# Optimization experiments

Hardware: AMD Instinct MI355X
Metric: run time of the kernel (lower is better)

The kernel has to match this reference:

```python
import jax, jax.numpy as jnp
import numpy as np

EPS = 1e-06
NUM_HEADS = 16


def _rms_norm(x, g, eps=EPS):
    # normalize over the last (full model) dim, as WanRMSNorm(dim)
    var = jnp.mean(jnp.square(x), axis=-1, keepdims=True)
    return x * jax.lax.rsqrt(var + eps) * g


def _apply_rope(q, k, freqs):
    # q, k: [b, s, n, d]; freqs: [s, d//2] angles. Interleaved (complex) pairs
    b, s, n, d = q.shape
    cos = jnp.cos(freqs)[None, :, None, :]  # [1, s, 1, d//2]
    sin = jnp.sin(freqs)[None, :, None, :]

    def rot(t):
        tr = t.reshape(b, s, n, d // 2, 2)
        t0, t1 = tr[..., 0], tr[..., 1]
        o0 = t0 * cos - t1 * sin
        o1 = t0 * sin + t1 * cos
        return jnp.stack([o0, o1], axis=-1).reshape(b, s, n, d)

    return rot(q), rot(k)


def setup_inputs() -> dict:
    key = jax.random.key(0)
    ks = jax.random.split(key, 8)
    b, s, dim = 2, 2048, 2048
    hd = dim // NUM_HEADS
    x = jax.random.normal(ks[0], (b, s, dim), dtype=jnp.float32)
    seq_lens = jax.random.randint(ks[1], (b,), s // 2, s + 1, dtype=jnp.int32)
    grid_sizes = jax.random.randint(ks[2], (b, 3), 1, 16).astype(jnp.int64)
    freqs = jax.random.uniform(ks[3], (s, hd // 2), dtype=jnp.float32) * 6.283
    sc = 1.0 / np.sqrt(dim)
    Wq = jax.random.normal(ks[4], (dim, dim), dtype=jnp.float32) * sc
    Wk = jax.random.normal(ks[5], (dim, dim), dtype=jnp.float32) * sc
    Wv = jax.random.normal(ks[6], (dim, dim), dtype=jnp.float32) * sc
    Wo = jax.random.normal(ks[7], (dim, dim), dtype=jnp.float32) * sc
    bo = jnp.zeros((dim,), dtype=jnp.float32)
    gq = jnp.ones((dim,), dtype=jnp.float32)
    gk = jnp.ones((dim,), dtype=jnp.float32)
    return {"x": x, "seq_lens": seq_lens, "grid_sizes": grid_sizes, "freqs": freqs,
            "Wq": Wq, "Wk": Wk, "Wv": Wv, "Wo": Wo, "bo": bo, "gq": gq, "gk": gk}


def reference(x, seq_lens, grid_sizes, freqs, Wq, Wk, Wv, Wo, bo, gq, gk):
    b, s, dim = x.shape
    n = NUM_HEADS
    d = dim // n
    scale = d ** (-0.5)

    # QKV projections (Linear: x @ W.T), with RMSNorm over full dim on q/k
    q = _rms_norm(x @ Wq.T, gq).reshape(b, s, n, d)
    k = _rms_norm(x @ Wk.T, gk).reshape(b, s, n, d)
    v = (x @ Wv.T).reshape(b, s, n, d)

    q, k = _apply_rope(q, k, freqs)

    # varlen attention: keys beyond seq_lens[b] are masked out
    scores = jnp.einsum("bqnd,bknd->bnqk", q, k) * scale
    key_valid = jnp.arange(s)[None, None, None, :] < seq_lens[:, None, None, None]
    scores = jnp.where(key_valid, scores, jnp.float32(-1e9))
    probs = jax.nn.softmax(scores, axis=-1)
    attn = jnp.einsum("bnqk,bknd->bqnd", probs, v).reshape(b, s, dim)

    return attn @ Wo.T + bo
```

## Files before the change

kernel.cpp:

```cpp
#include <hip/hip_runtime.h>
#include <hip/hip_bf16.h>
#include <math.h>

#define BATCH 2
#define SEQ   2048
#define DIM   2048
#define NH    16
#define HD    128
#define NROWS (BATCH * SEQ)
#define EPS_RMS 1e-6f

typedef unsigned short ushort_t;
typedef unsigned int   uint_t;
typedef __bf16    bf16x8 __attribute__((ext_vector_type(8)));
typedef _Float16  f16x8  __attribute__((ext_vector_type(8)));
typedef float     f32x4  __attribute__((ext_vector_type(4)));

__device__ inline ushort_t f2bf(float f) {
    uint_t u = __builtin_bit_cast(uint_t, f);
    uint_t r = u + 0x7FFFu + ((u >> 16) & 1u);
    return (ushort_t)(r >> 16);
}
__device__ inline ushort_t f2h(float f) {
    return __builtin_bit_cast(ushort_t, (_Float16)f);
}

__global__ __launch_bounds__(256) void cvt_all_kernel(
    const float* __restrict__ x,  const float* __restrict__ wq,
    const float* __restrict__ wk, const float* __restrict__ wv,
    const float* __restrict__ wo,
    ushort_t* __restrict__ xh,  ushort_t* __restrict__ wqh,
    ushort_t* __restrict__ wkh, ushort_t* __restrict__ wvh,
    ushort_t* __restrict__ woh)
{
    const int blk = blockIdx.x;
    const float* src; ushort_t* dst; size_t base;
    if (blk < 4096) { src = x; dst = xh; base = (size_t)blk * 2048; }
    else {
        const int r = blk - 4096;
        const int wsel = r >> 11;
        base = (size_t)(r & 2047) * 2048;
        if      (wsel == 0) { src = wq; dst = wqh; }
        else if (wsel == 1) { src = wk; dst = wkh; }
        else if (wsel == 2) { src = wv; dst = wvh; }
        else                { src = wo; dst = woh; }
    }
    const size_t i = base + ((size_t)threadIdx.x << 3);
    float v[8];
    *(float4*)&v[0] = *(const float4*)&src[i];
    *(float4*)&v[4] = *(const float4*)&src[i + 4];
    uint_t pk[4];
#pragma unroll
    for (int j = 0; j < 4; ++j)
        pk[j] = (uint_t)f2h(v[2 * j]) | ((uint_t)f2h(v[2 * j + 1]) << 16);
    *(uint4*)&dst[i] = make_uint4(pk[0], pk[1], pk[2], pk[3]);
}

template<int MODE>
__global__ __launch_bounds__(256, 2) void gemm_f16_kernel(
    const ushort_t* __restrict__ Ah, const ushort_t* __restrict__ Bh,
    const float* __restrict__ bias,
    float* __restrict__ C, ushort_t* __restrict__ Ct,
    const int M, const int N, const int K)
{
    __shared__ __align__(16) ushort_t sA[4096], sB[4096];
    const int tid  = threadIdx.x;
    const int w    = tid >> 6;
    const int lane = tid & 63;
    const int m0 = blockIdx.y * 128;
    const int n0 = blockIdx.x * 128;

    const int scol = (lane & 3) << 3;
    const int wr = w >> 1, wc = w & 1;
    const int fr = lane & 15, quad = lane >> 4;

    f32x4 acc[4][4];
#pragma unroll
    for (int mi = 0; mi < 4; ++mi)
#pragma unroll
        for (int ni = 0; ni < 4; ++ni)
            acc[mi][ni] = (f32x4){0.f, 0.f, 0.f, 0.f};

    for (int k0 = 0; k0 < K; k0 += 32) {
        __syncthreads();
#pragma unroll
        for (int it = 0; it < 2; ++it) {
            const int row  = (w << 5) + (it << 4) + (lane >> 2);
            const int loff = (w << 10) + (it << 9);
            const size_t ga = (size_t)(m0 + row) * K + k0 + scol;
            const size_t gb = (size_t)(n0 + row) * K + k0 + scol;
            __builtin_amdgcn_global_load_lds(
                (const __attribute__((address_space(1))) uint_t*)(const void*)(Ah + ga),
                (__attribute__((address_space(3))) uint_t*)(void*)&sA[loff], 16, 0, 0);
            __builtin_amdgcn_global_load_lds(
                (const __attribute__((address_space(1))) uint_t*)(const void*)(Bh + gb),
                (__attribute__((address_space(3))) uint_t*)(void*)&sB[loff], 16, 0, 0);
        }
        __syncthreads();

        f16x8 bfr[4];
#pragma unroll
        for (int ni = 0; ni < 4; ++ni) {
            const int row = (wc << 6) + (ni << 4) + fr;
            bfr[ni] = *(const f16x8*)&sB[(row << 5) + (quad << 3)];
        }
#pragma unroll
        for (int mi = 0; mi < 4; ++mi) {
            const int row = (wr << 6) + (mi << 4) + fr;
            const f16x8 ah = *(const f16x8*)&sA[(row << 5) + (quad << 3)];
#pragma unroll
            for (int ni = 0; ni < 4; ++ni)
                acc[mi][ni] = __builtin_amdgcn_mfma_f32_16x16x32_f16(ah, bfr[ni], acc[mi][ni], 0, 0, 0);
        }
    }

#pragma unroll
    for (int mi = 0; mi < 4; ++mi)
#pragma unroll
        for (int ni = 0; ni < 4; ++ni) {
            const int col = n0 + (wc << 6) + (ni << 4) + fr;
            if (MODE == 0) {
                const float bv = bias ? bias[col] : 0.f;
#pragma unroll
                for (int r = 0; r < 4; ++r) {
                    const int rowg = m0 + (wr << 6) + (mi << 4) + (quad << 2) + r;
                    C[(size_t)rowg * N + col] = acc[mi][ni][r] + bv;
                }
            } else {
                const int rowg = m0 + (wr << 6) + (mi << 4) + (quad << 2);
                const int bb = rowg >> 11, tok = rowg & (SEQ - 1);
                const int hh = col >> 7, d = col & (HD - 1);
                uint2 pk;
                pk.x = (uint_t)f2bf(acc[mi][ni][0]) | ((uint_t)f2bf(acc[mi][ni][1]) << 16);
                pk.y = (uint_t)f2bf(acc[mi][ni][2]) | ((uint_t)f2bf(acc[mi][ni][3]) << 16);
                *(uint2*)&Ct[((size_t)(bb * NH + hh) * HD + d) * SEQ + tok] = pk;
            }
        }
}

__global__ __launch_bounds__(256, 3) void qkv_gemm_kernel(
    const ushort_t* __restrict__ Ah, const ushort_t* __restrict__ Bq,
    const ushort_t* __restrict__ Bk, const ushort_t* __restrict__ Bv,
    float* __restrict__ Qb, float* __restrict__ Kb, ushort_t* __restrict__ Vt)
{
    __shared__ __align__(16) ushort_t sA[4096], sB[4096];
    const int tid  = threadIdx.x;
    const int w    = tid >> 6;
    const int lane = tid & 63;

    const int bid = blockIdx.x;
    const int nid = (bid & 7) * 192 + (bid >> 3);
    const int n_blk = nid >> 5;
    const int m_blk = nid & 31;
    const int wsel  = n_blk >> 4;
    const int m0 = m_blk * 128;
    const int n0 = (n_blk & 15) * 128;
    const ushort_t* __restrict__ Bh = (wsel == 0) ? Bq : (wsel == 1) ? Bk : Bv;

    const int scol = (lane & 3) << 3;
    const int wr = w >> 1, wc = w & 1;
    const int fr = lane & 15, quad = lane >> 4;

    f32x4 acc[4][4];
#pragma unroll
    for (int mi = 0; mi < 4; ++mi)
#pragma unroll
        for (int ni = 0; ni < 4; ++ni)
            acc[mi][ni] = (f32x4){0.f, 0.f, 0.f, 0.f};

    for (int k0 = 0; k0 < DIM; k0 += 32) {
        __syncthreads();
#pragma unroll
        for (int it = 0; it < 2; ++it) {
            const int row  = (w << 5) + (it << 4) + (lane >> 2);
            const int loff = (w << 10) + (it << 9);
            const size_t ga = (size_t)(m0 + row) * DIM + k0 + scol;
            const size_t gb = (size_t)(n0 + row) * DIM + k0 + scol;
            __builtin_amdgcn_global_load_lds(
                (const __attribute__((address_space(1))) uint_t*)(const void*)(Ah + ga),
                (__attribute__((address_space(3))) uint_t*)(void*)&sA[loff], 16, 0, 0);
            __builtin_amdgcn_global_load_lds(
                (const __attribute__((address_space(1))) uint_t*)(const void*)(Bh + gb),
                (__attribute__((address_space(3))) uint_t*)(void*)&sB[loff], 16, 0, 0);
        }
        __syncthreads();

        f16x8 bfr[4];
#pragma unroll
        for (int ni = 0; ni < 4; ++ni) {
            const int row = (wc << 6) + (ni << 4) + fr;
            bfr[ni] = *(const f16x8*)&sB[(row << 5) + (quad << 3)];
        }
#pragma unroll
        for (int mi = 0; mi < 4; ++mi) {
            const int row = (wr << 6) + (mi << 4) + fr;
            const f16x8 ah = *(const f16x8*)&sA[(row << 5) + (quad << 3)];
#pragma unroll
            for (int ni = 0; ni < 4; ++ni)
                acc[mi][ni] = __builtin_amdgcn_mfma_f32_16x16x32_f16(ah, bfr[ni], acc[mi][ni], 0, 0, 0);
        }
    }

    if (wsel < 2) {
        float* __restrict__ C = (wsel == 0) ? Qb : Kb;
#pragma unroll
        for (int mi = 0; mi < 4; ++mi)
#pragma unroll
            for (int ni = 0; ni < 4; ++ni) {
                const int col = n0 + (wc << 6) + (ni << 4) + fr;
#pragma unroll
                for (int r = 0; r < 4; ++r) {
                    const int rowg = m0 + (wr << 6) + (mi << 4) + (quad << 2) + r;
                    C[(size_t)rowg * DIM + col] = acc[mi][ni][r];
                }
            }
    } else {
#pragma unroll
        for (int mi = 0; mi < 4; ++mi)
#pragma unroll
            for (int ni = 0; ni < 4; ++ni) {
                const int col = n0 + (wc << 6) + (ni << 4) + fr;
                const int rowg = m0 + (wr << 6) + (mi << 4) + (quad << 2);
                const int bb = rowg >> 11, tok = rowg & (SEQ - 1);
                const int hh = col >> 7, d = col & (HD - 1);
                uint2 pk;
                pk.x = (uint_t)f2bf(acc[mi][ni][0]) | ((uint_t)f2bf(acc[mi][ni][1]) << 16);
                pk.y = (uint_t)f2bf(acc[mi][ni][2]) | ((uint_t)f2bf(acc[mi][ni][3]) << 16);
                *(uint2*)&Vt[((size_t)(bb * NH + hh) * HD + d) * SEQ + tok] = pk;
            }
    }
}

#define BM 64
#define BN 64
#define BK 16

__global__ __launch_bounds__(256) void gemm_nt_kernel(
    const float* __restrict__ A, const float* __restrict__ W,
    const float* __restrict__ bias, float* __restrict__ C,
    const int M, const int N, const int K)
{
    __shared__ float As[BK][BM + 4];
    __shared__ float Bs[BK][BN + 4];
    const int tid = threadIdx.x;
    const int tx = tid & 15;
    const int ty = tid >> 4;
    const int m0 = blockIdx.y * BM;
    const int n0 = blockIdx.x * BN;
    const int ldr = tid >> 2;
    const int ldc = (tid & 3) << 2;

    float acc[4][4] = {};

    for (int k0 = 0; k0 < K; k0 += BK) {
        __syncthreads();
        const float4 av = *(const float4*)&A[(size_t)(m0 + ldr) * K + (k0 + ldc)];
        const float4 wv = *(const float4*)&W[(size_t)(n0 + ldr) * K + (k0 + ldc)];
        As[ldc + 0][ldr] = av.x; As[ldc + 1][ldr] = av.y;
        As[ldc + 2][ldr] = av.z; As[ldc + 3][ldr] = av.w;
        Bs[ldc + 0][ldr] = wv.x; Bs[ldc + 1][ldr] = wv.y;
        Bs[ldc + 2][ldr] = wv.z; Bs[ldc + 3][ldr] = wv.w;
        __syncthreads();
#pragma unroll
        for (int k = 0; k < BK; ++k) {
            const float4 a4 = *(const float4*)&As[k][ty << 2];
            const float4 b4 = *(const float4*)&Bs[k][tx << 2];
            const float aa[4] = {a4.x, a4.y, a4.z, a4.w};
            const float bb[4] = {b4.x, b4.y, b4.z, b4.w};
#pragma unroll
            for (int i = 0; i < 4; ++i)
#pragma unroll
                for (int j = 0; j < 4; ++j)
                    acc[i][j] = fmaf(aa[i], bb[j], acc[i][j]);
        }
    }

#pragma unroll
    for (int i = 0; i < 4; ++i) {
        const int row = m0 + (ty << 2) + i;
        const int col = n0 + (tx << 2);
        float4 ov;
        ov.x = acc[i][0]; ov.y = acc[i][1]; ov.z = acc[i][2]; ov.w = acc[i][3];
        if (bias != nullptr) {
            ov.x += bias[col + 0]; ov.y += bias[col + 1];
            ov.z += bias[col + 2]; ov.w += bias[col + 3];
        }
        *(float4*)&C[(size_t)row * N + col] = ov;
    }
}

__global__ __launch_bounds__(256) void rmsnorm_rope_qk_kernel(
    const float* __restrict__ Qb, const float* __restrict__ gq,
    ushort_t* __restrict__ qbh,
    const float* __restrict__ Kb, const float* __restrict__ gk,
    ushort_t* __restrict__ kbh,
    const float* __restrict__ freqs)
{
    const int r = blockIdx.x;
    const int s = r & (SEQ - 1);
    const int tid = threadIdx.x;
    const int base = tid << 3;
    const bool isQ = (blockIdx.y == 0);
    const float* T = isQ ? Qb : Kb;
    const float* g = isQ ? gq : gk;
    ushort_t* out  = isQ ? qbh : kbh;
    const float posc = isQ ? 0.088388347648318447f : 1.0f;

    float v[8];
    *(float4*)&v[0] = *(const float4*)&T[(size_t)r * DIM + base];
    *(float4*)&v[4] = *(const float4*)&T[(size_t)r * DIM + base + 4];

    float ss = 0.f;
#pragma unroll
    for (int i = 0; i < 8; ++i) ss += v[i] * v[i];
#pragma unroll
    for (int off = 32; off > 0; off >>= 1) ss += __shfl_down(ss, off);

    __shared__ float wsum[4];
    __shared__ float inv_sh;
    if ((tid & 63) == 0) wsum[tid >> 6] = ss;
    __syncthreads();
    if (tid == 0)
        inv_sh = rsqrtf((wsum[0] + wsum[1] + wsum[2] + wsum[3]) * (1.0f / DIM) + EPS_RMS);
    __syncthreads();
    const float inv = inv_sh * posc;

    float gg[8];
    *(float4*)&gg[0] = *(const float4*)&g[base];
    *(float4*)&gg[4] = *(const float4*)&g[base + 4];
#pragma unroll
    for (int i = 0; i < 8; ++i) v[i] *= inv * gg[i];

    const int p0 = (base & (HD - 1)) >> 1;
#pragma unroll
    for (int pp = 0; pp < 4; ++pp) {
        float sn, cs;
        __sincosf(freqs[(size_t)s * (HD / 2) + p0 + pp], &sn, &cs);
        const float t0 = v[2 * pp], t1 = v[2 * pp + 1];
        v[2 * pp]     = t0 * cs - t1 * sn;
        v[2 * pp + 1] = t0 * sn + t1 * cs;
    }

    uint_t pk[4];
#pragma unroll
    for (int j = 0; j < 4; ++j)
        pk[j] = (uint_t)f2bf(v[2 * j]) | ((uint_t)f2bf(v[2 * j + 1]) << 16);
    *(uint4*)&out[(size_t)r * DIM + base] = make_uint4(pk[0], pk[1], pk[2], pk[3]);
}

__global__ __launch_bounds__(256) void rmsnorm_rope_kernel(
    float* __restrict__ T, const float* __restrict__ g,
    const float* __restrict__ freqs)
{
    const int r = blockIdx.x;
    const int s = r & (SEQ - 1);
    const int tid = threadIdx.x;
    const int base = tid << 3;

    float v[8];
    *(float4*)&v[0] = *(const float4*)&T[(size_t)r * DIM + base];
    *(float4*)&v[4] = *(const float4*)&T[(size_t)r * DIM + base + 4];

    float ss = 0.f;
#pragma unroll
    for (int i = 0; i < 8; ++i) ss += v[i] * v[i];
#pragma unroll
    for (int off = 32; off > 0; off >>= 1) ss += __shfl_down(ss, off);

    __shared__ float wsum[4];
    __shared__ float inv_sh;
    if ((tid & 63) == 0) wsum[tid >> 6] = ss;
    __syncthreads();
    if (tid == 0)
        inv_sh = rsqrtf((wsum[0] + wsum[1] + wsum[2] + wsum[3]) * (1.0f / DIM) + EPS_RMS);
    __syncthreads();
    const float inv = inv_sh;

    float gg[8];
    *(float4*)&gg[0] = *(const float4*)&g[base];
    *(float4*)&gg[4] = *(const float4*)&g[base + 4];
#pragma unroll
    for (int i = 0; i < 8; ++i) v[i] *= inv * gg[i];

    const int p0 = (base & (HD - 1)) >> 1;
#pragma unroll
    for (int pp = 0; pp < 4; ++pp) {
        float sn, cs;
        __sincosf(freqs[(size_t)s * (HD / 2) + p0 + pp], &sn, &cs);
        const float t0 = v[2 * pp], t1 = v[2 * pp + 1];
        v[2 * pp]     = t0 * cs - t1 * sn;
        v[2 * pp + 1] = t0 * sn + t1 * cs;
    }

    *(float4*)&T[(size_t)r * DIM + base]     = *(float4*)&v[0];
    *(float4*)&T[(size_t)r * DIM + base + 4] = *(float4*)&v[4];
}

#define AQ 128
#define AK 64
#define KSTR 136
#define VSTR 72
#define RESCALE_THR 8.0f

__global__ __launch_bounds__(256, 2) void attn_mfma_kernel(
    const ushort_t* __restrict__ QH, const ushort_t* __restrict__ KH,
    const ushort_t* __restrict__ VtG, const int* __restrict__ seq_lens,
    ushort_t* __restrict__ Oh)
{
    __shared__ __align__(16) ushort_t sK[AK * KSTR];
    __shared__ __align__(16) ushort_t sVt[HD * VSTR];
    __shared__ __align__(16) ushort_t sP[AQ * VSTR];

    const int tid  = threadIdx.x;
    const int w    = tid >> 6;
    const int lane = tid & 63;
    const int fr   = lane & 15;
    const int quad = lane >> 4;
    const int q0   = blockIdx.x * AQ;
    const int h    = blockIdx.y;
    const int b    = blockIdx.z;
    const int len  = seq_lens[b];

    bf16x8 qfrag[2][4];
#pragma unroll
    for (int qt = 0; qt < 2; ++qt)
#pragma unroll
        for (int h4 = 0; h4 < 4; ++h4) {
            const size_t qrow = (size_t)(b * SEQ + q0 + (w << 5) + (qt << 4) + fr);
            qfrag[qt][h4] = *(const bf16x8*)&QH[qrow * DIM + h * HD + (h4 << 5) + (quad << 3)];
        }

    f32x4 Oacc[2][8];
#pragma unroll
    for (int qt = 0; qt < 2; ++qt)
#pragma unroll
        for (int dt = 0; dt < 8; ++dt)
            Oacc[qt][dt] = (f32x4){0.f, 0.f, 0.f, 0.f};
    float mrow[2] = {-1.0e30f, -1.0e30f};
    float lrow[2] = {0.f, 0.f};

    const int ntiles = (len + AK - 1) / AK;
    for (int t = 0; t < ntiles; ++t) {
        const int k0 = t * AK;
        const bool masked = (k0 + AK > len);
        __syncthreads();
        for (int i = tid; i < AK * 16; i += 256) {
            const int key = i >> 4, c8 = (i & 15) << 3;
            const uint4 kv = *(const uint4*)&KH[(size_t)(b * SEQ + k0 + key) * DIM + h * HD + c8];
            *(uint4*)&sK[key * KSTR + c8] = kv;
        }
        for (int i = tid; i < HD * 8; i += 256) {
            const int d = i >> 3, kc = (i & 7) << 3;
            const uint4 vv = *(const uint4*)&VtG[((size_t)(b * NH + h) * HD + d) * SEQ + k0 + kc];
            *(uint4*)&sVt[d * VSTR + kc] = vv;
        }
        __syncthreads();

        f32x4 S[4][2];
        __builtin_amdgcn_s_setprio(1);
#pragma unroll
        for (int kt = 0; kt < 4; ++kt) {
            bf16x8 kf[4];
#pragma unroll
            for (int h4 = 0; h4 < 4; ++h4)
                kf[h4] = *(const bf16x8*)&sK[((kt << 4) + fr) * KSTR + (h4 << 5) + (quad << 3)];
#pragma unroll
            for (int qt = 0; qt < 2; ++qt) {
                f32x4 a = (f32x4){0.f, 0.f, 0.f, 0.f};
#pragma unroll
                for (int h4 = 0; h4 < 4; ++h4)
                    a = __builtin_amdgcn_mfma_f32_16x16x32_bf16(kf[h4], qfrag[qt][h4], a, 0, 0, 0);
                S[kt][qt] = a;
            }
        }
        __builtin_amdgcn_s_setprio(0);

#pragma unroll
        for (int qt = 0; qt < 2; ++qt) {
            float tm = -1.0e30f;
            if (masked) {
#pragma unroll
                for (int kt = 0; kt < 4; ++kt)
#pragma unroll
                    for (int r = 0; r < 4; ++r) {
                        const int key = k0 + (kt << 4) + (quad << 2) + r;
                        float s = (key < len) ? S[kt][qt][r] : -1.0e30f;
                        S[kt][qt][r] = s;
                        tm = fmaxf(tm, s);
                    }
            } else {
#pragma unroll
                for (int kt = 0; kt < 4; ++kt)
#pragma unroll
                    for (int r = 0; r < 4; ++r)
                        tm = fmaxf(tm, S[kt][qt][r]);
            }
            tm = fmaxf(tm, __shfl_xor(tm, 16));
            tm = fmaxf(tm, __shfl_xor(tm, 32));

            float mnew;
            if (__all(tm - mrow[qt] <= RESCALE_THR)) {
                mnew = mrow[qt];
            } else {
                mnew = fmaxf(mrow[qt], tm);
                const float alpha = __expf(mrow[qt] - mnew);
                mrow[qt] = mnew;
                lrow[qt] *= alpha;
#pragma unroll
                for (int r = 0; r < 4; ++r) {
                    const float ar = __shfl(alpha, (quad << 2) + r);
#pragma unroll
                    for (int dt = 0; dt < 8; ++dt)
                        Oacc[qt][dt][r] *= ar;
                }
            }

            float rsum = 0.f;
#pragma unroll
            for (int kt = 0; kt < 4; ++kt) {
                float p[4];
#pragma unroll
                for (int r = 0; r < 4; ++r) {
                    p[r] = __expf(S[kt][qt][r] - mnew);
                    rsum += p[r];
                }
                uint2 pk;
                pk.x = (uint_t)f2bf(p[0]) | ((uint_t)f2bf(p[1]) << 16);
                pk.y = (uint_t)f2bf(p[2]) | ((uint_t)f2bf(p[3]) << 16);
                *(uint2*)&sP[((w << 5) + (qt << 4) + fr) * VSTR + (kt << 4) + (quad << 2)] = pk;
            }
            rsum += __shfl_xor(rsum, 16);
            rsum += __shfl_xor(rsum, 32);
            lrow[qt] += rsum;
        }

        __builtin_amdgcn_s_setprio(1);
#pragma unroll
        for (int ks = 0; ks < 2; ++ks) {
            bf16x8 pf[2];
#pragma unroll
            for (int qt = 0; qt < 2; ++qt)
                pf[qt] = *(const bf16x8*)&sP[((w << 5) + (qt << 4) + fr) * VSTR + (ks << 5) + (quad << 3)];
#pragma unroll
            for (int dt = 0; dt < 8; ++dt) {
                const bf16x8 vf = *(const bf16x8*)&sVt[((dt << 4) + fr) * VSTR + (ks << 5) + (quad << 3)];
#pragma unroll
                for (int qt = 0; qt < 2; ++qt)
                    Oacc[qt][dt] = __builtin_amdgcn_mfma_f32_16x16x32_bf16(pf[qt], vf, Oacc[qt][dt], 0, 0, 0);
            }
        }
        __builtin_amdgcn_s_setprio(0);
    }

#pragma unroll
    for (int qt = 0; qt < 2; ++qt) {
        float linv[4];
#pragma unroll
        for (int r = 0; r < 4; ++r)
            linv[r] = 1.0f / __shfl(lrow[qt], (quad << 2) + r);
#pragma unroll
        for (int dt = 0; dt < 8; ++dt)
#pragma unroll
            for (int r = 0; r < 4; ++r) {
                const int qrow = q0 + (w << 5) + (qt << 4) + (quad << 2) + r;
                Oh[(size_t)(b * SEQ + qrow) * DIM + h * HD + (dt << 4) + fr] =
                    f2h(Oacc[qt][dt][r] * linv[r]);
            }
    }
}

#define BQ  64
#define BKT 64

__global__ __launch_bounds__(256) void attn_kernel(
    const float* __restrict__ Q, const float* __restrict__ K,
    const float* __restrict__ V, const int* __restrict__ seq_lens,
    float* __restrict__ O)
{
    const int qt = blockIdx.x;
    const int h  = blockIdx.y;
    const int b  = blockIdx.z;
    const int len = seq_lens[b];
    const int q0 = qt * BQ;
    const float scale = 0.088388347648318447f;

    __shared__ float Qst[HD][BQ + 4];
    __shared__ float Kst[HD][BKT + 4];
    __shared__ float Vs[BKT][HD + 4];
    __shared__ float Sc[BQ][BKT + 1];
    __shared__ float mrow[BQ], lrow[BQ], alpha_s[BQ];

    const int tid = threadIdx.x;
    const int si0 = (tid >> 4) << 2;
    const int sj0 = (tid & 15) << 2;
    const int pi0 = (tid >> 4) << 2;
    const int pc0 = (tid & 15) << 3;

    for (int i = tid; i < BQ * HD / 4; i += 256) {
        const int e = i << 2;
        const int row = e >> 7;
        const int c0 = e & (HD - 1);
        const float4 qv = *(const float4*)&Q[(size_t)(b * SEQ + q0 + row) * DIM + h * HD + c0];
        Qst[c0 + 0][row] = qv.x; Qst[c0 + 1][row] = qv.y;
        Qst[c0 + 2][row] = qv.z; Qst[c0 + 3][row] = qv.w;
    }
    if (tid < BQ) { mrow[tid] = -3.0e38f; lrow[tid] = 0.f; }

    float o[4][8] = {};
    __syncthreads();

    const int ntiles = (len + BKT - 1) / BKT;
    for (int t = 0; t < ntiles; ++t) {
        const int k0 = t * BKT;
        __syncthreads();
        for (int i = tid; i < BKT * HD / 4; i += 256) {
            const int e = i << 2;
            const int row = e >> 7;
            const int c0 = e & (HD - 1);
            const int kg = k0 + row;
            float4 kv = make_float4(0.f, 0.f, 0.f, 0.f);
            float4 vv = make_float4(0.f, 0.f, 0.f, 0.f);
            if (kg < len) {
                kv = *(const float4*)&K[(size_t)(b * SEQ + kg) * DIM + h * HD + c0];
                vv = *(const float4*)&V[(size_t)(b * SEQ + kg) * DIM + h * HD + c0];
            }
            Kst[c0 + 0][row] = kv.x; Kst[c0 + 1][row] = kv.y;
            Kst[c0 + 2][row] = kv.z; Kst[c0 + 3][row] = kv.w;
            *(float4*)&Vs[row][c0] = vv;
        }
        __syncthreads();

        float acc[4][4] = {};
#pragma unroll 8
        for (int kk = 0; kk < HD; ++kk) {
            const float4 q4 = *(const float4*)&Qst[kk][si0];
            const float4 k4 = *(const float4*)&Kst[kk][sj0];
            const float qa[4] = {q4.x, q4.y, q4.z, q4.w};
            const float ka[4] = {k4.x, k4.y, k4.z, k4.w};
#pragma unroll
            for (int i = 0; i < 4; ++i)
#pragma unroll
                for (int j = 0; j < 4; ++j)
                    acc[i][j] = fmaf(qa[i], ka[j], acc[i][j]);
        }
#pragma unroll
        for (int i = 0; i < 4; ++i)
#pragma unroll
            for (int j = 0; j < 4; ++j) {
                const int jg = k0 + sj0 + j;
                Sc[si0 + i][sj0 + j] = (jg < len) ? acc[i][j] * scale : -1.0e9f;
            }
        __syncthreads();

        if (tid < BQ) {
            const int i = tid;
            const float m_old = mrow[i];
            float mx = m_old;
            for (int j = 0; j < BKT; ++j) mx = fmaxf(mx, Sc[i][j]);
            const float al = __expf(m_old - mx);
            float sum = 0.f;
            for (int j = 0; j < BKT; ++j) {
                const float p = __expf(Sc[i][j] - mx);
                Sc[i][j] = p;
                sum += p;
            }
            mrow[i] = mx;
            lrow[i] = lrow[i] * al + sum;
            alpha_s[i] = al;
        }
        __syncthreads();

#pragma unroll
        for (int i = 0; i < 4; ++i) {
            const float al = alpha_s[pi0 + i];
#pragma unroll
            for (int c = 0; c < 8; ++c) o[i][c] *= al;
        }
        for (int j = 0; j < BKT; ++j) {
            float p[4];
#pragma unroll
            for (int i = 0; i < 4; ++i) p[i] = Sc[pi0 + i][j];
            const float4 v0 = *(const float4*)&Vs[j][pc0];
            const float4 v1 = *(const float4*)&Vs[j][pc0 + 4];
            const float va[8] = {v0.x, v0.y, v0.z, v0.w, v1.x, v1.y, v1.z, v1.w};
#pragma unroll
            for (int i = 0; i < 4; ++i)
#pragma unroll
                for (int c = 0; c < 8; ++c)
                    o[i][c] = fmaf(p[i], va[c], o[i][c]);
        }
    }

#pragma unroll
    for (int i = 0; i < 4; ++i) {
        const float invl = 1.0f / lrow[pi0 + i];
        float4 w0, w1;
        w0.x = o[i][0] * invl; w0.y = o[i][1] * invl;
        w0.z = o[i][2] * invl; w0.w = o[i][3] * invl;
        w1.x = o[i][4] * invl; w1.y = o[i][5] * invl;
        w1.z = o[i][6] * invl; w1.w = o[i][7] * invl;
        float* op = &O[(size_t)(b * SEQ + q0 + pi0 + i) * DIM + h * HD + pc0];
        *(float4*)&op[0] = w0;
        *(float4*)&op[4] = w1;
    }
}

extern "C" void kernel_launch(void* const* d_in, const int* in_sizes, int n_in,
                              void* d_out, int out_size, void* d_ws, size_t ws_size,
                              hipStream_t stream)
{
    const float* x        = (const float*)d_in[0];
    const int*   seq_lens = (const int*)d_in[1];
    const float* freqs    = (const float*)d_in[3];
    const float* Wq       = (const float*)d_in[4];
    const float* Wk       = (const float*)d_in[5];
    const float* Wv       = (const float*)d_in[6];
    const float* Wo       = (const float*)d_in[7];
    const float* bo       = (const float*)d_in[8];
    const float* gq       = (const float*)d_in[9];
    const float* gk       = (const float*)d_in[10];
    float* out = (float*)d_out;

    const size_t mat = (size_t)NROWS * DIM;
    const size_t wsz = (size_t)DIM * DIM;

    float*    Qb   = (float*)d_ws;
    float*    Kb   = Qb + mat;
    ushort_t* xh   = (ushort_t*)(Kb + mat);
    ushort_t* wqh  = xh + mat;
    ushort_t* wkh  = wqh + wsz;
    ushort_t* wvh  = wkh + wsz;
    ushort_t* woh  = wvh + wsz;
    ushort_t* qbh  = woh + wsz;
    ushort_t* kbh  = qbh + mat;
    ushort_t* vtg  = kbh + mat;
    ushort_t* abh  = vtg + mat;

    const size_t need = 2 * mat * sizeof(float)
                      + (mat + 4 * wsz + 4 * mat) * sizeof(ushort_t);

    if (ws_size >= need) {
        cvt_all_kernel<<<12288, 256, 0, stream>>>(
            x, Wq, Wk, Wv, Wo, xh, wqh, wkh, wvh, woh);

        qkv_gemm_kernel<<<1536, 256, 0, stream>>>(xh, wqh, wkh, wvh, Qb, Kb, vtg);

        rmsnorm_rope_qk_kernel<<<dim3(NROWS, 2), 256, 0, stream>>>(
            Qb, gq, qbh, Kb, gk, kbh, freqs);

        attn_mfma_kernel<<<dim3(SEQ / AQ, NH, BATCH), 256, 0, stream>>>(qbh, kbh, vtg, seq_lens, abh);

        const dim3 gg(DIM / 128, NROWS / 128);
        gemm_f16_kernel<0><<<gg, 256, 0, stream>>>(abh, woh, bo, out, nullptr, NROWS, DIM, DIM);
    } else {
        float* Vb = Kb + mat;
        float* Ab = Vb + mat;
        const dim3 gemm_grid(DIM / BN, NROWS / BM);
        gemm_nt_kernel<<<gemm_grid, 256, 0, stream>>>(x, Wq, nullptr, Qb, NROWS, DIM, DIM);
        gemm_nt_kernel<<<gemm_grid, 256, 0, stream>>>(x, Wk, nullptr, Kb, NROWS, DIM, DIM);
        gemm_nt_kernel<<<gemm_grid, 256, 0, stream>>>(x, Wv, nullptr, Vb, NROWS, DIM, DIM);
        rmsnorm_rope_kernel<<<NROWS, 256, 0, stream>>>(Qb, gq, freqs);
        rmsnorm_rope_kernel<<<NROWS, 256, 0, stream>>>(Kb, gk, freqs);
        attn_kernel<<<dim3(SEQ / BQ, NH, BATCH), 256, 0, stream>>>(Qb, Kb, Vb, seq_lens, Ab);
        gemm_nt_kernel<<<gemm_grid, 256, 0, stream>>>(Ab, Wo, bo, out, NROWS, DIM, DIM);
    }
}
```

Baseline: 512.0 us.

## Prefetch next K/V tile into registers and swizzle attention block order

The attention kernel now loads the next K and V tiles from global memory into registers while the current tile is being computed, then writes them to shared memory at the start of the next iteration. This hides global load latency behind the MFMA work. The grid becomes 1D with a swizzle that maps consecutive block ids across different (q-block, head, batch) groups, with the intent of spreading work across XCDs and caches. The cost is extra registers per thread, which may pressure occupancy under launch_bounds(256,2).

```diff
diff --git a/kernel.cpp b/kernel.cpp
--- a/kernel.cpp
+++ b/kernel.cpp
@@ -416,10 +416,14 @@
     const int lane = tid & 63;
     const int fr   = lane & 15;
     const int quad = lane >> 4;
-    const int q0   = blockIdx.x * AQ;
-    const int h    = blockIdx.y;
-    const int b    = blockIdx.z;
-    const int len  = seq_lens[b];
+
+    const int bid = blockIdx.x;
+    const int sw  = (bid & 7) * 64 + (bid >> 3);
+    const int q0  = (sw & 15) * AQ;
+    const int hb  = sw >> 4;
+    const int h   = hb & 15;
+    const int b   = hb >> 4;
+    const int len = seq_lens[b];
 
     bf16x8 qfrag[2][4];
 #pragma unroll
@@ -439,22 +443,42 @@
     float mrow[2] = {-1.0e30f, -1.0e30f};
     float lrow[2] = {0.f, 0.f};
 
+    const int kr  = tid >> 4;
+    const int kc8 = (tid & 15) << 3;
+    const int vd  = tid >> 3;
+    const int vc8 = (tid & 7) << 3;
+    const size_t kbase = (size_t)(b * SEQ) * DIM + h * HD + kc8;
+    const size_t vbase = ((size_t)(b * NH + h) * HD) * SEQ + vc8;
+
+    uint4 kreg[4], vreg[4];
+#define LOAD_TILE(K0)                                                              \
+    {                                                                              \
+        _Pragma("unroll")                                                          \
+        for (int j = 0; j < 4; ++j)                                                \
+            kreg[j] = *(const uint4*)&KH[kbase + (size_t)((K0) + kr + (j << 4)) * DIM]; \
+        _Pragma("unroll")                                                          \
+        for (int j = 0; j < 4; ++j)                                                \
+            vreg[j] = *(const uint4*)&VtG[vbase + (size_t)(vd + (j << 5)) * SEQ + (K0)]; \
+    }
+#define STORE_TILE()                                                               \
+    {                                                                              \
+        _Pragma("unroll")                                                          \
+        for (int j = 0; j < 4; ++j)                                                \
+            *(uint4*)&sK[(kr + (j << 4)) * KSTR + kc8] = kreg[j];                  \
+        _Pragma("unroll")                                                          \
+        for (int j = 0; j < 4; ++j)                                                \
+            *(uint4*)&sVt[(vd + (j << 5)) * VSTR + vc8] = vreg[j];                 \
+    }
+
     const int ntiles = (len + AK - 1) / AK;
+    LOAD_TILE(0);
     for (int t = 0; t < ntiles; ++t) {
         const int k0 = t * AK;
         const bool masked = (k0 + AK > len);
         __syncthreads();
-        for (int i = tid; i < AK * 16; i += 256) {
-            const int key = i >> 4, c8 = (i & 15) << 3;
-            const uint4 kv = *(const uint4*)&KH[(size_t)(b * SEQ + k0 + key) * DIM + h * HD + c8];
-            *(uint4*)&sK[key * KSTR + c8] = kv;
-        }
-        for (int i = tid; i < HD * 8; i += 256) {
-            const int d = i >> 3, kc = (i & 7) << 3;
-            const uint4 vv = *(const uint4*)&VtG[((size_t)(b * NH + h) * HD + d) * SEQ + k0 + kc];
-            *(uint4*)&sVt[d * VSTR + kc] = vv;
-        }
-        __syncthreads();
+        STORE_TILE();
+        __syncthreads();
+        if (t + 1 < ntiles) LOAD_TILE((t + 1) * AK);
 
         f32x4 S[4][2];
         __builtin_amdgcn_s_setprio(1);
@@ -551,6 +575,8 @@
         }
         __builtin_amdgcn_s_setprio(0);
     }
+#undef LOAD_TILE
+#undef STORE_TILE
 
 #pragma unroll
     for (int qt = 0; qt < 2; ++qt) {
@@ -748,7 +774,7 @@
         rmsnorm_rope_qk_kernel<<<dim3(NROWS, 2), 256, 0, stream>>>(
             Qb, gq, qbh, Kb, gk, kbh, freqs);
 
-        attn_mfma_kernel<<<dim3(SEQ / AQ, NH, BATCH), 256, 0, stream>>>(qbh, kbh, vtg, seq_lens, abh);
+        attn_mfma_kernel<<<512, 256, 0, stream>>>(qbh, kbh, vtg, seq_lens, abh);
 
         const dim3 gg(DIM / 128, NROWS / 128);
         gemm_f16_kernel<0><<<gg, 256, 0, stream>>>(abh, woh, bo, out, nullptr, NROWS, DIM, DIM);
```

Result: no change. 516.9 us (+1.0%).
